# Performance work log

Hardware: AMD Instinct MI355X
Metric: run time of the kernel (lower is better)

The kernel has to match this reference:

```python
import jax, jax.numpy as jnp
import numpy as np

B, T, D, U = 32, 2048, 512, 512


def setup_inputs() -> dict:
    key = jax.random.key(0)
    ks = jax.random.split(key, 6)
    scale = 0.05
    return {
        "values": jax.random.normal(ks[0], (B, T, D), dtype=jnp.float32),
        "query": jax.random.normal(ks[1], (B, D), dtype=jnp.float32),
        "W1_w": jax.random.normal(ks[2], (D, U), dtype=jnp.float32) * scale,
        "W1_b": jnp.zeros((U,), dtype=jnp.float32),
        "W2_w": jax.random.normal(ks[3], (D, U), dtype=jnp.float32) * scale,
        "W2_b": jnp.zeros((U,), dtype=jnp.float32),
        "V_w": jax.random.normal(ks[4], (U, 1), dtype=jnp.float32) * scale,
        "V_b": jnp.zeros((1,), dtype=jnp.float32),
    }


def reference(values, query, W1_w, W1_b, W2_w, W2_b, V_w, V_b):
    # values: [B, T, D]; query: [B, D]
    proj_v = jnp.einsum("btd,du->btu", values, W1_w) + W1_b          # [B, T, U]
    proj_q = (query @ W2_w + W2_b)[:, None, :]                        # [B, 1, U]
    score = jnp.tanh(proj_v + proj_q) @ V_w + V_b                     # [B, T, 1]
    attention_weights = jax.nn.softmax(score, axis=1)                 # [B, T, 1]
    context_vector = jnp.sum(attention_weights * values, axis=1)      # [B, D]
    return context_vector, attention_weights
```

## Files before the change

### kernel.cpp

```cpp
#include <hip/hip_runtime.h>
#include <hip/hip_bf16.h>
#include <stdint.h>


#define B_DIM 32
#define T_DIM 2048
#define D_DIM 512
#define U_DIM 512
#define M_DIM (B_DIM * T_DIM)

typedef short bf16x8 __attribute__((ext_vector_type(8)));
typedef float f32x4 __attribute__((ext_vector_type(4)));

__device__ __forceinline__ float fast_tanh(float x) {
    float e = __expf(2.0f * x);
    return 1.0f - __fdividef(2.0f, e + 1.0f);
}

__device__ __forceinline__ short bf16r(float x) {
    unsigned u = __float_as_uint(x);
    u += 0x7fffu + ((u >> 16) & 1u);
    return (short)(u >> 16);
}

__device__ __forceinline__ bf16x8 pack8v(f32x4 a, f32x4 b) {
    union { __hip_bfloat162 h[4]; bf16x8 v; } u;
    u.h[0] = __float22bfloat162_rn(make_float2(a[0], a[1]));
    u.h[1] = __float22bfloat162_rn(make_float2(a[2], a[3]));
    u.h[2] = __float22bfloat162_rn(make_float2(b[0], b[1]));
    u.h[3] = __float22bfloat162_rn(make_float2(b[2], b[3]));
    return u.v;
}


__global__ void prep_kernel(const float* __restrict__ W1_w,
                            const float* __restrict__ W1_b,
                            const float* __restrict__ W2_w,
                            const float* __restrict__ W2_b,
                            const float* __restrict__ query,
                            unsigned short* __restrict__ W1T,
                            float* __restrict__ qb) {
    __shared__ float red[256];
    const int tid = threadIdx.x;
    if (blockIdx.x < 128) {
        int n = blockIdx.x * 256 + tid;
        int uu    = n & 255;
        int kc    = (n >> 8) & 3;
        int kstep = (n >> 10) & 15;
        int ut    = n >> 14;
        int u  = ut * 256 + uu;
        int k0 = kstep * 32 + kc * 8;
        bf16x8 pk;
#pragma unroll
        for (int j = 0; j < 8; ++j)
            pk[j] = bf16r(W1_w[(size_t)(k0 + j) * U_DIM + u]);
        ((bf16x8*)W1T)[n] = pk;
    } else {
        int bid = blockIdx.x - 128;
        int b  = bid >> 3;
        int ug = bid & 7;
        int u  = ug * 64 + (tid & 63);
        int dq = tid >> 6;
        const float* q  = query + b * D_DIM + dq * 128;
        const float* w2 = W2_w + (size_t)(dq * 128) * U_DIM + u;
        float acc = 0.f;
#pragma unroll 8
        for (int d = 0; d < 128; ++d)
            acc += q[d] * w2[(size_t)d * U_DIM];
        red[tid] = acc;
        __syncthreads();
        if (tid < 64) {
            qb[b * U_DIM + u] = red[tid] + red[tid + 64] + red[tid + 128]
                              + red[tid + 192] + W2_b[u] + W1_b[u];
        }
    }
}

__global__ __launch_bounds__(512, 4) void fused_kernel(
        const float* __restrict__ values,
        const unsigned short* __restrict__ W1T,
        const float* __restrict__ qb,
        const float* __restrict__ Vw,
        float* __restrict__ sP,
        float* __restrict__ Pms,
        float* __restrict__ Pctx) {
    __shared__ float sred[4][64];
    __shared__ float ew[64];
    __shared__ __align__(16) float red[4][512];

    const int tid  = threadIdx.x;
    const int lane = tid & 63;
    const int w    = tid >> 6;
    const int l15  = lane & 15;
    const int quad = lane >> 4;
    const int wr   = w >> 2;
    const int wc   = w & 3;
    const int chunk = blockIdx.x;
    const int mb   = chunk * 64;
    const int b    = mb >> 11;

    const float* arow0 = values + (size_t)(mb + wr * 32 + l15) * D_DIM + quad * 8;
    const float* arow1 = arow0 + 16 * D_DIM;
    const unsigned short* bbase =
        W1T + ((size_t)(wc >> 1) * 16384 + quad * 256 + (wc & 1) * 128 + l15) * 8;

    f32x4 acc[2][8] = {};

#pragma unroll 1
    for (int ks = 0; ks < 16; ++ks) {
        const unsigned short* bks = bbase + (size_t)ks * 8192;
        bf16x8 bfr[8];
#pragma unroll
        for (int ui = 0; ui < 8; ++ui)
            bfr[ui] = *(const bf16x8*)(bks + (size_t)ui * 128);

        f32x4 a00 = *(const f32x4*)(arow0 + ks * 32);
        f32x4 a01 = *(const f32x4*)(arow0 + ks * 32 + 4);
        f32x4 a10 = *(const f32x4*)(arow1 + ks * 32);
        f32x4 a11 = *(const f32x4*)(arow1 + ks * 32 + 4);

        bf16x8 a0 = pack8v(a00, a01);
        bf16x8 a1 = pack8v(a10, a11);
        __builtin_amdgcn_s_setprio(1);
#pragma unroll
        for (int ui = 0; ui < 8; ++ui) {
            acc[0][ui] = __builtin_amdgcn_mfma_f32_16x16x32_bf16(a0, bfr[ui], acc[0][ui], 0, 0, 0);
            acc[1][ui] = __builtin_amdgcn_mfma_f32_16x16x32_bf16(a1, bfr[ui], acc[1][ui], 0, 0, 0);
        }
        __builtin_amdgcn_s_setprio(0);
    }

    const int ub = wc * 128 + l15;
    float sm[2][4] = {};
#pragma unroll
    for (int ui = 0; ui < 8; ++ui) {
        const int u = ub + ui * 16;
        const float qv = qb[b * U_DIM + u];
        const float vw = Vw[u];
#pragma unroll
        for (int mt = 0; mt < 2; ++mt)
#pragma unroll
            for (int r = 0; r < 4; ++r)
                sm[mt][r] += fast_tanh(acc[mt][ui][r] + qv) * vw;
    }
#pragma unroll
    for (int mt = 0; mt < 2; ++mt)
#pragma unroll
        for (int r = 0; r < 4; ++r) {
            float v = sm[mt][r];
            v += __shfl_xor(v, 1, 64);
            v += __shfl_xor(v, 2, 64);
            v += __shfl_xor(v, 4, 64);
            v += __shfl_xor(v, 8, 64);
            sm[mt][r] = v;
        }
    if (l15 == 0) {
#pragma unroll
        for (int mt = 0; mt < 2; ++mt)
#pragma unroll
            for (int r = 0; r < 4; ++r)
                sred[wc][wr * 32 + mt * 16 + quad * 4 + r] = sm[mt][r];
    }
    __syncthreads();

    if (tid < 64) {
        float s = sred[0][tid] + sred[1][tid] + sred[2][tid] + sred[3][tid];
        sP[mb + tid] = s;
        float m = s;
#pragma unroll
        for (int off = 1; off < 64; off <<= 1)
            m = fmaxf(m, __shfl_xor(m, off, 64));
        float e = __expf(s - m);
        ew[tid] = e;
        float S = e;
#pragma unroll
        for (int off = 1; off < 64; off <<= 1)
            S += __shfl_xor(S, off, 64);
        if (tid == 0) { Pms[chunk * 2] = m; Pms[chunk * 2 + 1] = S; }
    }
    __syncthreads();

    {
        const int d4 = tid & 127;
        const int th = tid >> 7;
        const float4* vb = (const float4*)(values + (size_t)(mb + th * 16) * D_DIM) + d4;
        float4 a = {0.f, 0.f, 0.f, 0.f};
#pragma unroll
        for (int i = 0; i < 16; ++i) {
            float e = ew[th * 16 + i];
            float4 v = vb[(size_t)i * 128];
            a.x += e * v.x; a.y += e * v.y;
            a.z += e * v.z; a.w += e * v.w;
        }
        ((float4*)red)[th * 128 + d4] = a;
    }
    __syncthreads();
    if (tid < 128) {
        float4 o0 = ((float4*)red)[tid];
        float4 o1 = ((float4*)red)[128 + tid];
        float4 o2 = ((float4*)red)[256 + tid];
        float4 o3 = ((float4*)red)[384 + tid];
        float4 o;
        o.x = o0.x + o1.x + o2.x + o3.x;
        o.y = o0.y + o1.y + o2.y + o3.y;
        o.z = o0.z + o1.z + o2.z + o3.z;
        o.w = o0.w + o1.w + o2.w + o3.w;
        *(float4*)(Pctx + (size_t)chunk * 512 + tid * 4) = o;
    }
}

__global__ void combine_kernel(const float* __restrict__ Pctx,
                               const float* __restrict__ Pms,
                               const float* __restrict__ sP,
                               float* __restrict__ out) {
    __shared__ float sc[32];
    const int b   = blockIdx.x;
    const int tid = threadIdx.x;

    float m = -1e30f;
#pragma unroll
    for (int c = 0; c < 32; ++c)
        m = fmaxf(m, Pms[(b * 32 + c) * 2]);
    if (tid < 32) sc[tid] = __expf(Pms[(b * 32 + tid) * 2] - m);
    __syncthreads();
    float S = 0.f;
#pragma unroll
    for (int c = 0; c < 32; ++c)
        S += sc[c] * Pms[(b * 32 + c) * 2 + 1];
    const float invS = 1.0f / S;

#pragma unroll
    for (int h = 0; h < 2; ++h) {
        const int d = h * 256 + tid;
        float a = 0.f;
#pragma unroll
        for (int c = 0; c < 32; ++c)
            a += sc[c] * Pctx[(size_t)(b * 32 + c) * 512 + d];
        out[b * D_DIM + d] = a * invS;
    }
#pragma unroll
    for (int j = 0; j < 8; ++j) {
        const int g = b * T_DIM + j * 256 + tid;
        out[B_DIM * D_DIM + g] = __expf(sP[g] - m) * invS;
    }
}

extern "C" void kernel_launch(void* const* d_in, const int* in_sizes, int n_in,
                              void* d_out, int out_size, void* d_ws, size_t ws_size,
                              hipStream_t stream) {
    const float* values = (const float*)d_in[0];
    const float* query  = (const float*)d_in[1];
    const float* W1_w   = (const float*)d_in[2];
    const float* W1_b   = (const float*)d_in[3];
    const float* W2_w   = (const float*)d_in[4];
    const float* W2_b   = (const float*)d_in[5];
    const float* V_w    = (const float*)d_in[6];

    float* out = (float*)d_out;

    unsigned char* ws = (unsigned char*)d_ws;
    unsigned short* W1T = (unsigned short*)(ws);
    float* qb  = (float*)(ws + 524288);
    float* sP  = (float*)(ws + 589824);
    float* Pms = (float*)(ws + 851968);
    float* Pctx= (float*)(ws + 860160);

    prep_kernel<<<384, 256, 0, stream>>>(W1_w, W1_b, W2_w, W2_b, query, W1T, qb);
    fused_kernel<<<1024, 512, 0, stream>>>(values, W1T, qb, V_w, sP, Pms, Pctx);
    combine_kernel<<<B_DIM, 256, 0, stream>>>(Pctx, Pms, sP, out);
}
```

Measured before the change: 296.2 us.

## Stage bf16-converted values tile in swizzled LDS and widen combine grid

The fused kernel now loads the block's 64x512 fp32 values tile once with coalesced loads. It converts the tile to bf16 and stores it in a XOR-swizzled 64KB shared buffer, and the MFMA loop reads A fragments from there. Previously each wave loaded and converted A from global memory redundantly across column waves. The combine kernel is split into 256 smaller blocks holding per-thread exp weights to increase parallelism. The added 64KB of LDS reduces blocks per CU, and the tile load is no longer overlapped with compute.

Result: faster. 274.1 us (-7.5%).

```diff
diff --git a/kernel.cpp b/kernel.cpp
--- a/kernel.cpp
+++ b/kernel.cpp
@@ -21,15 +21,6 @@
     unsigned u = __float_as_uint(x);
     u += 0x7fffu + ((u >> 16) & 1u);
     return (short)(u >> 16);
-}
-
-__device__ __forceinline__ bf16x8 pack8v(f32x4 a, f32x4 b) {
-    union { __hip_bfloat162 h[4]; bf16x8 v; } u;
-    u.h[0] = __float22bfloat162_rn(make_float2(a[0], a[1]));
-    u.h[1] = __float22bfloat162_rn(make_float2(a[2], a[3]));
-    u.h[2] = __float22bfloat162_rn(make_float2(b[0], b[1]));
-    u.h[3] = __float22bfloat162_rn(make_float2(b[2], b[3]));
-    return u.v;
 }
 
 
@@ -84,6 +75,7 @@
         float* __restrict__ sP,
         float* __restrict__ Pms,
         float* __restrict__ Pctx) {
+    __shared__ __align__(16) unsigned char Abuf[65536];
     __shared__ float sred[4][64];
     __shared__ float ew[64];
     __shared__ __align__(16) float red[4][512];
@@ -99,10 +91,27 @@
     const int mb   = chunk * 64;
     const int b    = mb >> 11;
 
-    const float* arow0 = values + (size_t)(mb + wr * 32 + l15) * D_DIM + quad * 8;
-    const float* arow1 = arow0 + 16 * D_DIM;
+    {
+        const float* src = values + (size_t)mb * D_DIM;
+#pragma unroll 4
+        for (int it = 0; it < 16; ++it) {
+            int idx = it * 2048 + tid * 4;
+            f32x4 v = *(const f32x4*)(src + idx);
+            int row = idx >> 9;
+            int k   = idx & 511;
+            union { __hip_bfloat162 h[2]; unsigned long long u; } pk;
+            pk.h[0] = __float22bfloat162_rn(make_float2(v[0], v[1]));
+            pk.h[1] = __float22bfloat162_rn(make_float2(v[2], v[3]));
+            int addr = row * 1024 + ((((k >> 3) ^ (row & 7)) << 4) | ((k & 7) * 2));
+            *(unsigned long long*)(Abuf + addr) = pk.u;
+        }
+    }
+    __syncthreads();
+
     const unsigned short* bbase =
         W1T + ((size_t)(wc >> 1) * 16384 + quad * 256 + (wc & 1) * 128 + l15) * 8;
+    const int r0 = wr * 32 + l15;
+    const int r1 = r0 + 16;
 
     f32x4 acc[2][8] = {};
 
@@ -114,13 +123,10 @@
         for (int ui = 0; ui < 8; ++ui)
             bfr[ui] = *(const bf16x8*)(bks + (size_t)ui * 128);
 
-        f32x4 a00 = *(const f32x4*)(arow0 + ks * 32);
-        f32x4 a01 = *(const f32x4*)(arow0 + ks * 32 + 4);
-        f32x4 a10 = *(const f32x4*)(arow1 + ks * 32);
-        f32x4 a11 = *(const f32x4*)(arow1 + ks * 32 + 4);
-
-        bf16x8 a0 = pack8v(a00, a01);
-        bf16x8 a1 = pack8v(a10, a11);
+        const int slot = ks * 4 + quad;
+        bf16x8 a0 = *(const bf16x8*)(Abuf + r0 * 1024 + ((slot ^ (r0 & 7)) << 4));
+        bf16x8 a1 = *(const bf16x8*)(Abuf + r1 * 1024 + ((slot ^ (r1 & 7)) << 4));
+
         __builtin_amdgcn_s_setprio(1);
 #pragma unroll
         for (int ui = 0; ui < 8; ++ui) {
@@ -213,34 +219,35 @@
                                const float* __restrict__ Pms,
                                const float* __restrict__ sP,
                                float* __restrict__ out) {
-    __shared__ float sc[32];
-    const int b   = blockIdx.x;
+    const int bid = blockIdx.x;
+    const int b   = bid >> 3;
+    const int p   = bid & 7;
     const int tid = threadIdx.x;
 
     float m = -1e30f;
 #pragma unroll
     for (int c = 0; c < 32; ++c)
         m = fmaxf(m, Pms[(b * 32 + c) * 2]);
-    if (tid < 32) sc[tid] = __expf(Pms[(b * 32 + tid) * 2] - m);
-    __syncthreads();
+    float ec[32];
     float S = 0.f;
 #pragma unroll
-    for (int c = 0; c < 32; ++c)
-        S += sc[c] * Pms[(b * 32 + c) * 2 + 1];
+    for (int c = 0; c < 32; ++c) {
+        ec[c] = __expf(Pms[(b * 32 + c) * 2] - m);
+        S += ec[c] * Pms[(b * 32 + c) * 2 + 1];
+    }
     const float invS = 1.0f / S;
 
-#pragma unroll
-    for (int h = 0; h < 2; ++h) {
-        const int d = h * 256 + tid;
+    {
+        const int d = p * 64 + tid;
         float a = 0.f;
 #pragma unroll
         for (int c = 0; c < 32; ++c)
-            a += sc[c] * Pctx[(size_t)(b * 32 + c) * 512 + d];
+            a += ec[c] * Pctx[(size_t)(b * 32 + c) * 512 + d];
         out[b * D_DIM + d] = a * invS;
     }
 #pragma unroll
-    for (int j = 0; j < 8; ++j) {
-        const int g = b * T_DIM + j * 256 + tid;
+    for (int j = 0; j < 4; ++j) {
+        const int g = b * T_DIM + p * 256 + j * 64 + tid;
         out[B_DIM * D_DIM + g] = __expf(sP[g] - m) * invS;
     }
 }
@@ -267,5 +274,5 @@
 
     prep_kernel<<<384, 256, 0, stream>>>(W1_w, W1_b, W2_w, W2_b, query, W1T, qb);
     fused_kernel<<<1024, 512, 0, stream>>>(values, W1T, qb, V_w, sP, Pms, Pctx);
-    combine_kernel<<<B_DIM, 256, 0, stream>>>(Pctx, Pms, sP, out);
-}
+    combine_kernel<<<256, 64, 0, stream>>>(Pctx, Pms, sP, out);
+}
```
